# Kernel optimization log

Hardware: AMD Instinct MI355X
Metric: run time of the kernel (lower is better)

## Reference

```python
import jax, jax.numpy as jnp
import numpy as np

N_NODES = 40000
N_EDGES = 150000
H, D = 4, 128  # heads, per-head dim (h_feats=512)


def _edge_softmax(e, dst, n):
    # e: [E, H] attention logits; softmax over edges sharing a dst node
    m = jax.ops.segment_max(e, dst, num_segments=n)
    w = jnp.exp(e - m[dst])
    s = jax.ops.segment_sum(w, dst, num_segments=n)
    return w / s[dst]


def _gat_conv(x, src, dst, W, al, ar, b, activate):
    # DGL GATConv: feat = x @ W -> [N, H, D]
    n = x.shape[0]
    feat = (x @ W).reshape(n, H, D)
    el = jnp.einsum('nhd,hd->nh', feat, al)  # [N, H]
    er = jnp.einsum('nhd,hd->nh', feat, ar)
    e = jax.nn.leaky_relu(el[src] + er[dst], negative_slope=0.2)  # [E, H]
    a = _edge_softmax(e, dst, n)
    msg = feat[src] * a[:, :, None]  # [E, H, D]
    out = jax.ops.segment_sum(msg, dst, num_segments=n)  # [N, H, D]
    out = out + b.reshape(1, H, D)
    if activate:
        out = jax.nn.leaky_relu(out, negative_slope=0.01)  # F.leaky_relu default
    return out


def _hetero_layer(h, edges, W, al, ar, b, activate):
    # HeteroGraphConv with aggregate='sum' over edge types, then flatten heads
    n = h.shape[0]
    out = jnp.zeros((n, H, D), h.dtype)
    for t, (src, dst) in enumerate(edges):
        out = out + _gat_conv(h, src, dst, W[t], al[t], ar[t], b[t], activate)
    return out.reshape(n, H * D)


def setup_inputs() -> dict:
    key = jax.random.key(0)
    ks = jax.random.split(key, 20)
    inp = {}
    inp['x'] = jax.random.normal(ks[0], (N_NODES, 1024), jnp.float32)
    for i, nm in enumerate(['src0', 'dst0', 'src1', 'dst1']):
        inp[nm] = jax.random.randint(ks[1 + i], (N_EDGES,), 0, N_NODES, jnp.int32)
    def wscale(k, shape, fan_in):
        return jax.random.normal(k, shape, jnp.float32) * (1.0 / np.sqrt(fan_in))
    inp['W0'] = wscale(ks[5], (2, 1024, 512), 1024)
    inp['al0'] = wscale(ks[6], (2, H, D), D)
    inp['ar0'] = wscale(ks[7], (2, H, D), D)
    inp['b0'] = jnp.zeros((2, 512), jnp.float32)
    inp['W1'] = wscale(ks[8], (2, 512, 512), 512)
    inp['al1'] = wscale(ks[9], (2, H, D), D)
    inp['ar1'] = wscale(ks[10], (2, H, D), D)
    inp['b1'] = jnp.zeros((2, 512), jnp.float32)
    inp['W2'] = wscale(ks[11], (2, 512, 512), 512)
    inp['al2'] = wscale(ks[12], (2, H, D), D)
    inp['ar2'] = wscale(ks[13], (2, H, D), D)
    inp['b2'] = jnp.zeros((2, 512), jnp.float32)
    inp['Wout'] = wscale(ks[14], (512, 2983), 512)
    inp['bout'] = jnp.zeros((2983,), jnp.float32)
    return inp


def reference(x, src0, dst0, src1, dst1,
              W0, al0, ar0, b0, W1, al1, ar1, b1, W2, al2, ar2, b2,
              Wout, bout):
    edges = [(src0, dst0), (src1, dst1)]
    h = _hetero_layer(x, edges, W0, al0, ar0, b0, activate=True)
    h = _hetero_layer(h, edges, W1, al1, ar1, b1, activate=True)
    h = _hetero_layer(h, edges, W2, al2, ar2, b2, activate=False)
    return h @ Wout + bout
```

## Files before the change

kernel.cpp:

```cpp
#include <hip/hip_runtime.h>
#include <hip/hip_bf16.h>

#define NN 40000
#define NE 150000
#define HF 512
#define NHEAD 4

typedef __bf16 bf16x8 __attribute__((ext_vector_type(8)));
typedef float floatx4 __attribute__((ext_vector_type(4)));
typedef __hip_bfloat16 bf16;
typedef unsigned short u16;

__device__ __forceinline__ float bf2f(bf16 v) { return __bfloat162float(v); }
__device__ __forceinline__ float u2f(u16 v) { return __uint_as_float(((unsigned)v) << 16); }

__device__ __forceinline__ void gload16(const void* g, void* l) {
    __builtin_amdgcn_global_load_lds(
        (const __attribute__((address_space(1))) void*)g,
        (__attribute__((address_space(3))) void*)l, 16, 0, 0);
}

__device__ __forceinline__ void wait_vm0() {
    asm volatile("s_waitcnt vmcnt(0)" ::: "memory");
}

__device__ __forceinline__ void store_c(float* p, float v) { *p = v; }
__device__ __forceinline__ void store_c(bf16* p, float v) { *p = __float2bfloat16(v); }

__global__ void cast_k(const float* __restrict__ in, bf16* __restrict__ out, int n) {
    int i = (blockIdx.x * blockDim.x + threadIdx.x) * 8;
    if (i + 7 < n) {
        float4 v0 = *(const float4*)(in + i);
        float4 v1 = *(const float4*)(in + i + 4);
        union { uint4 u; u16 s[8]; } w;
        float fv[8] = {v0.x, v0.y, v0.z, v0.w, v1.x, v1.y, v1.z, v1.w};
#pragma unroll
        for (int j = 0; j < 8; j++) {
            bf16 b = __float2bfloat16(fv[j]);
            w.s[j] = *(const u16*)&b;
        }
        *(uint4*)(out + i) = w.u;
    } else {
        for (int j = i; j < n; j++) out[j] = __float2bfloat16(in[j]);
    }
}

__global__ void transpose_k(const float* __restrict__ W, bf16* __restrict__ WT,
                            int K, int Nn) {
    __shared__ float tile[32][33];
    int n0 = blockIdx.x * 32, k0 = blockIdx.y * 32;
    int tx = threadIdx.x, ty = threadIdx.y;
    int n = n0 + tx, k = k0 + ty;
    if (n < Nn && k < K) tile[ty][tx] = W[(size_t)k * Nn + n];
    __syncthreads();
    int nn = n0 + ty, kk = k0 + tx;
    if (nn < Nn && kk < K) WT[(size_t)nn * K + kk] = __float2bfloat16(tile[tx][ty]);
}

template <typename TOUT, bool HAS_BIAS>
__global__ __launch_bounds__(256) void gemm_k(const bf16* __restrict__ A,
                                              const bf16* __restrict__ BT,
                                              TOUT* __restrict__ C,
                                              const float* __restrict__ bias,
                                              int M, int Nn, int K) {
    __shared__ __align__(16) unsigned short As[2][128][32];
    __shared__ __align__(16) unsigned short Bs[2][128][32];

    const int nwg = gridDim.x * gridDim.y;
    const int orig = blockIdx.y * gridDim.x + blockIdx.x;
    const int qq = nwg >> 3, r8 = nwg & 7;
    const int xcd = orig & 7, loc = orig >> 3;
    const int swz = (xcd < r8 ? xcd * (qq + 1) : r8 * (qq + 1) + (xcd - r8) * qq) + loc;
    const int ntile = swz % gridDim.x;
    const int mtile = swz / gridDim.x;
    const int m0 = mtile * 128;
    const int n0 = ntile * 128;

    const int t = threadIdx.x;
    const int lane = t & 63;
    const int wave = t >> 6;
    const int wm = wave >> 1, wn = wave & 1;
    const int q = lane >> 4, r = lane & 15;

    const int srow = wave * 32 + (lane >> 2);
    const int scol = ((lane & 3) ^ ((srow >> 1) & 3)) * 8;
    int ar0 = m0 + srow;        if (ar0 >= M)  ar0 = M - 1;
    int ar1 = m0 + srow + 16;   if (ar1 >= M)  ar1 = M - 1;
    int br0 = n0 + srow;        if (br0 >= Nn) br0 = Nn - 1;
    int br1 = n0 + srow + 16;   if (br1 >= Nn) br1 = Nn - 1;
    const unsigned short* Ag0 = (const unsigned short*)A + (size_t)ar0 * K + scol;
    const unsigned short* Ag1 = (const unsigned short*)A + (size_t)ar1 * K + scol;
    const unsigned short* Bg0 = (const unsigned short*)BT + (size_t)br0 * K + scol;
    const unsigned short* Bg1 = (const unsigned short*)BT + (size_t)br1 * K + scol;
    unsigned short* Alb[2] = {&As[0][0][0] + wave * 1024, &As[1][0][0] + wave * 1024};
    unsigned short* Blb[2] = {&Bs[0][0][0] + wave * 1024, &Bs[1][0][0] + wave * 1024};

    const int rchunk = (q ^ ((r >> 1) & 3)) * 8;

    floatx4 acc[4][4] = {};
    const int nt = K >> 5;
    int cur = 0;
    gload16(Ag0, Alb[0]);
    gload16(Ag1, Alb[0] + 512);
    gload16(Bg0, Blb[0]);
    gload16(Bg1, Blb[0] + 512);
    wait_vm0();
    __syncthreads();
    for (int tt = 0; tt < nt; tt++) {
        if (tt + 1 < nt) {
            const int k1 = (tt + 1) << 5;
            gload16(Ag0 + k1, Alb[cur ^ 1]);
            gload16(Ag1 + k1, Alb[cur ^ 1] + 512);
            gload16(Bg0 + k1, Blb[cur ^ 1]);
            gload16(Bg1 + k1, Blb[cur ^ 1] + 512);
        }
        bf16x8 a[4], b[4];
#pragma unroll
        for (int i = 0; i < 4; i++)
            a[i] = *(const bf16x8*)&As[cur][wm * 64 + i * 16 + r][rchunk];
#pragma unroll
        for (int j = 0; j < 4; j++)
            b[j] = *(const bf16x8*)&Bs[cur][wn * 64 + j * 16 + r][rchunk];
#pragma unroll
        for (int i = 0; i < 4; i++)
#pragma unroll
            for (int j = 0; j < 4; j++)
                acc[i][j] = __builtin_amdgcn_mfma_f32_16x16x32_bf16(a[i], b[j], acc[i][j], 0, 0, 0);
        wait_vm0();
        __syncthreads();
        cur ^= 1;
    }

    float bv4[4] = {0.f, 0.f, 0.f, 0.f};
    if (HAS_BIAS) {
#pragma unroll
        for (int j = 0; j < 4; j++) {
            int col = n0 + wn * 64 + j * 16 + r;
            if (col < Nn) bv4[j] = bias[col];
        }
    }
#pragma unroll
    for (int i = 0; i < 4; i++)
#pragma unroll
        for (int j = 0; j < 4; j++)
#pragma unroll
            for (int rr = 0; rr < 4; rr++) {
                int row = m0 + wm * 64 + i * 16 + q * 4 + rr;
                int col = n0 + wn * 64 + j * 16 + r;
                if (row < M && col < Nn) {
                    float v = acc[i][j][rr];
                    if (HAS_BIAS) v += bv4[j];
                    store_c(&C[(size_t)row * Nn + col], v);
                }
            }
}

__global__ void attn_k(const bf16* __restrict__ featb, const float* __restrict__ al_l,
                       const float* __restrict__ ar_l, float* __restrict__ el,
                       float* __restrict__ er) {
    int lane = threadIdx.x & 63;
    int wave = threadIdx.x >> 6;
    int node = blockIdx.x * 4 + wave;
    if (node >= NN) return;
    int tt = lane >> 5, h = (lane >> 3) & 3, ld = lane & 7;
    const u16* fp = (const u16*)featb + (size_t)node * 1024 + lane * 16;
    union { uint4 v; u16 s[8]; } u0, u1;
    u0.v = *(const uint4*)fp;
    u1.v = *(const uint4*)(fp + 8);
    const float* alp = al_l + tt * HF + h * 128 + ld * 16;
    const float* arp = ar_l + tt * HF + h * 128 + ld * 16;
    float sl = 0.f, sr = 0.f;
#pragma unroll
    for (int j = 0; j < 8; j++) {
        float f = u2f(u0.s[j]);
        sl += f * alp[j];
        sr += f * arp[j];
    }
#pragma unroll
    for (int j = 0; j < 8; j++) {
        float f = u2f(u1.s[j]);
        sl += f * alp[8 + j];
        sr += f * arp[8 + j];
    }
#pragma unroll
    for (int off = 4; off >= 1; off >>= 1) {
        sl += __shfl_down(sl, off, 8);
        sr += __shfl_down(sr, off, 8);
    }
    if (ld == 0) {
        size_t o = (size_t)tt * NN * NHEAD + node * NHEAD + h;
        el[o] = sl;
        er[o] = sr;
    }
}

__global__ void deg_count_k(const int* __restrict__ dst, int* __restrict__ deg) {
    int e = blockIdx.x * blockDim.x + threadIdx.x;
    if (e < NE) atomicAdd(&deg[dst[e]], 1);
}

__global__ void scan_k(const int* __restrict__ deg, int* __restrict__ off) {
    __shared__ int part[1024];
    const int CH = (NN + 1023) >> 10;
    int t = threadIdx.x;
    int base = t * CH;
    int s = 0;
    for (int i = 0; i < CH; i++) {
        int idx = base + i;
        if (idx < NN) s += deg[idx];
    }
    part[t] = s;
    __syncthreads();
    for (int d = 1; d < 1024; d <<= 1) {
        int v = (t >= d) ? part[t - d] : 0;
        __syncthreads();
        part[t] += v;
        __syncthreads();
    }
    int run = (t == 0) ? 0 : part[t - 1];
    for (int i = 0; i < CH; i++) {
        int idx = base + i;
        if (idx < NN) {
            off[idx] = run;
            run += deg[idx];
        } else if (idx == NN) {
            off[NN] = run;
        }
    }
}

__global__ void fill_k(const int* __restrict__ src, const int* __restrict__ dst,
                       const int* __restrict__ off, int* __restrict__ cur,
                       int* __restrict__ csrc) {
    int e = blockIdx.x * blockDim.x + threadIdx.x;
    if (e >= NE) return;
    int d = dst[e];
    int p = atomicAdd(&cur[d], 1);
    csrc[off[d] + p] = src[e];
}

__global__ __launch_bounds__(256) void gather_k(
    const int* __restrict__ off0, const int* __restrict__ csrc0,
    const int* __restrict__ off1, const int* __restrict__ csrc1,
    const float* __restrict__ el, const float* __restrict__ er,
    const bf16* __restrict__ featb, const float* __restrict__ bb_l,
    bf16* __restrict__ hout, int act) {
    int lane = threadIdx.x & 63;
    int wave = threadIdx.x >> 6;
    int d = blockIdx.x * 4 + wave;
    if (d >= NN) return;
    int h = lane >> 4;
    const int* offs[2] = {off0, off1};
    const int* csrcs[2] = {csrc0, csrc1};

    float out[8] = {};
#pragma unroll
    for (int tt = 0; tt < 2; tt++) {
        const int* off = offs[tt];
        const int* csrc = csrcs[tt];
        const float* elt = el + (size_t)tt * NN * NHEAD;
        int o0 = off[d], o1 = off[d + 1];
        float erd = er[(size_t)tt * NN * NHEAD + d * NHEAD + h];
        float m = -3.0e38f, sum = 0.f;
        for (int i = o0; i < o1; i++) {
            int s = csrc[i];
            float lg = elt[s * NHEAD + h] + erd;
            lg = lg > 0.f ? lg : 0.2f * lg;
            float mn = fmaxf(m, lg);
            sum = sum * __expf(m - mn) + __expf(lg - mn);
            m = mn;
        }
        float inv = sum > 0.f ? 1.f / sum : 0.f;
        float acc[8] = {};
        for (int i = o0; i < o1; i++) {
            int s = csrc[i];
            float lg = elt[s * NHEAD + h] + erd;
            lg = lg > 0.f ? lg : 0.2f * lg;
            float a = __expf(lg - m) * inv;
            const u16* fp = (const u16*)featb + (size_t)s * 1024 + tt * HF + lane * 8;
            union { uint4 v; u16 s8[8]; } u;
            u.v = *(const uint4*)fp;
#pragma unroll
            for (int j = 0; j < 8; j++) acc[j] += u2f(u.s8[j]) * a;
        }
        const float* bp = bb_l + tt * HF + lane * 8;
        float4 b0 = *(const float4*)bp;
        float4 b1 = *(const float4*)(bp + 4);
        float bv[8] = {b0.x, b0.y, b0.z, b0.w, b1.x, b1.y, b1.z, b1.w};
#pragma unroll
        for (int j = 0; j < 8; j++) {
            float v = acc[j] + bv[j];
            if (act) v = v > 0.f ? v : 0.01f * v;
            out[j] += v;
        }
    }
    union { uint4 v; u16 s[8]; } outw;
#pragma unroll
    for (int j = 0; j < 8; j++) {
        bf16 ob = __float2bfloat16(out[j]);
        outw.s[j] = *(const u16*)&ob;
    }
    *(uint4*)((u16*)hout + (size_t)d * HF + lane * 8) = outw.v;
}

extern "C" void kernel_launch(void* const* d_in, const int* in_sizes, int n_in,
                              void* d_out, int out_size, void* d_ws, size_t ws_size,
                              hipStream_t stream) {
    const float* x = (const float*)d_in[0];
    const int* srcs[2] = {(const int*)d_in[1], (const int*)d_in[3]};
    const int* dsts[2] = {(const int*)d_in[2], (const int*)d_in[4]};
    const float* W[3] = {(const float*)d_in[5], (const float*)d_in[9], (const float*)d_in[13]};
    const float* al[3] = {(const float*)d_in[6], (const float*)d_in[10], (const float*)d_in[14]};
    const float* ar[3] = {(const float*)d_in[7], (const float*)d_in[11], (const float*)d_in[15]};
    const float* bb[3] = {(const float*)d_in[8], (const float*)d_in[12], (const float*)d_in[16]};
    const float* Wout = (const float*)d_in[17];
    const float* bout = (const float*)d_in[18];

    char* ws = (char*)d_ws;
    size_t off = 0;
    auto walloc = [&](size_t bytes) {
        void* p = ws + off;
        off = (off + bytes + 255) & ~(size_t)255;
        return p;
    };
    bf16* h0 = (bf16*)walloc((size_t)NN * HF * 2);
    bf16* h1 = (bf16*)walloc((size_t)NN * HF * 2);
    float* el = (float*)walloc((size_t)2 * NN * NHEAD * 4);
    float* er = (float*)walloc((size_t)2 * NN * NHEAD * 4);
    bf16* WT = (bf16*)walloc((size_t)2983 * 512 * 2);
    bf16* WT2 = (bf16*)walloc((size_t)1024 * 1024 * 2);
    int* deg = (int*)walloc((size_t)NN * 4);
    int* cur = (int*)walloc((size_t)NN * 4);
    int* offs[2];
    int* csrc[2];
    for (int t = 0; t < 2; t++) {
        offs[t] = (int*)walloc((size_t)(NN + 1) * 4);
        csrc[t] = (int*)walloc((size_t)NE * 4);
    }

    bf16* xb = (bf16*)((char*)d_out + (size_t)NN * HF * 4);
    bf16* featb = (bf16*)((char*)d_out + (size_t)NN * HF * 4 + (size_t)NN * 1024 * 2);

    cast_k<<<(NN * 1024 / 8 + 255) / 256, 256, 0, stream>>>(x, xb, NN * 1024);

    const int EB = (NE + 255) / 256;
    for (int t = 0; t < 2; t++) {
        hipMemsetAsync(deg, 0, (size_t)NN * 4, stream);
        hipMemsetAsync(cur, 0, (size_t)NN * 4, stream);
        deg_count_k<<<EB, 256, 0, stream>>>(dsts[t], deg);
        scan_k<<<1, 1024, 0, stream>>>(deg, offs[t]);
        fill_k<<<EB, 256, 0, stream>>>(srcs[t], dsts[t], offs[t], cur, csrc[t]);
    }

    const int MT = (NN + 127) / 128;

    for (int l = 0; l < 3; l++) {
        const int K = (l == 0) ? 1024 : 512;
        const bf16* hin = (l == 0) ? xb : ((l == 1) ? h0 : h1);
        bf16* hout = (l == 0) ? h0 : ((l == 1) ? h1 : h0);
        const int act = (l < 2) ? 1 : 0;
        for (int t = 0; t < 2; t++)
            transpose_k<<<dim3(512 / 32, K / 32), dim3(32, 32), 0, stream>>>(
                W[l] + (size_t)t * K * 512, WT2 + (size_t)t * 512 * K, K, 512);
        gemm_k<bf16, false><<<dim3(1024 / 128, MT), 256, 0, stream>>>(
            hin, WT2, featb, nullptr, NN, 1024, K);
        attn_k<<<NN / 4, 256, 0, stream>>>(featb, al[l], ar[l], el, er);
        gather_k<<<NN / 4, 256, 0, stream>>>(offs[0], csrc[0], offs[1], csrc[1],
                                             el, er, featb, bb[l], hout, act);
    }

    transpose_k<<<dim3((2983 + 31) / 32, 512 / 32), dim3(32, 32), 0, stream>>>(
        Wout, WT, 512, 2983);
    gemm_k<float, true><<<dim3((2983 + 127) / 128, MT), 256, 0, stream>>>(
        h0, WT, (float*)d_out, bout, NN, 2983, 512);
}
```

Before: 1.578 ms.

## Triple-buffer GEMM LDS tiles with partial vmcnt waits and nontemporal float stores

Turns the GEMM main loop from double to triple buffering. Loads are now issued two K-tiles ahead, and the loop waits only until the older tile has arrived (vmcnt(4)) instead of draining all loads each iteration. This aims to hide global-memory latency behind the MFMA work. It also switches float output stores to nontemporal stores to reduce cache pollution, at the cost of 50% more LDS per block, which may lower occupancy.

Result: slower. 1.726 ms (+9.4%).

```diff
diff --git a/kernel.cpp b/kernel.cpp
--- a/kernel.cpp
+++ b/kernel.cpp
@@ -20,11 +20,9 @@
         (__attribute__((address_space(3))) void*)l, 16, 0, 0);
 }
 
-__device__ __forceinline__ void wait_vm0() {
-    asm volatile("s_waitcnt vmcnt(0)" ::: "memory");
-}
-
-__device__ __forceinline__ void store_c(float* p, float v) { *p = v; }
+__device__ __forceinline__ void store_c(float* p, float v) {
+    __builtin_nontemporal_store(v, p);
+}
 __device__ __forceinline__ void store_c(bf16* p, float v) { *p = __float2bfloat16(v); }
 
 __global__ void cast_k(const float* __restrict__ in, bf16* __restrict__ out, int n) {
@@ -63,8 +61,8 @@
                                               TOUT* __restrict__ C,
                                               const float* __restrict__ bias,
                                               int M, int Nn, int K) {
-    __shared__ __align__(16) unsigned short As[2][128][32];
-    __shared__ __align__(16) unsigned short Bs[2][128][32];
+    __shared__ __align__(16) unsigned short As[3][128][32];
+    __shared__ __align__(16) unsigned short Bs[3][128][32];
 
     const int nwg = gridDim.x * gridDim.y;
     const int orig = blockIdx.y * gridDim.x + blockIdx.x;
@@ -92,27 +90,34 @@
     const unsigned short* Ag1 = (const unsigned short*)A + (size_t)ar1 * K + scol;
     const unsigned short* Bg0 = (const unsigned short*)BT + (size_t)br0 * K + scol;
     const unsigned short* Bg1 = (const unsigned short*)BT + (size_t)br1 * K + scol;
-    unsigned short* Alb[2] = {&As[0][0][0] + wave * 1024, &As[1][0][0] + wave * 1024};
-    unsigned short* Blb[2] = {&Bs[0][0][0] + wave * 1024, &Bs[1][0][0] + wave * 1024};
 
     const int rchunk = (q ^ ((r >> 1) & 3)) * 8;
+
+    unsigned short* Abase = &As[0][0][0] + wave * 1024;
+    unsigned short* Bbase = &Bs[0][0][0] + wave * 1024;
+
+    auto STAGE = [&](int kk, int buf) {
+        const int k1 = kk << 5;
+        unsigned short* Al = Abase + buf * 4096;
+        unsigned short* Bl = Bbase + buf * 4096;
+        gload16(Ag0 + k1, Al);
+        gload16(Ag1 + k1, Al + 512);
+        gload16(Bg0 + k1, Bl);
+        gload16(Bg1 + k1, Bl + 512);
+    };
 
     floatx4 acc[4][4] = {};
     const int nt = K >> 5;
+    STAGE(0, 0);
+    STAGE(1, 1);
+    asm volatile("s_waitcnt vmcnt(4)" ::: "memory");
+    __builtin_amdgcn_s_barrier();
     int cur = 0;
-    gload16(Ag0, Alb[0]);
-    gload16(Ag1, Alb[0] + 512);
-    gload16(Bg0, Blb[0]);
-    gload16(Bg1, Blb[0] + 512);
-    wait_vm0();
-    __syncthreads();
     for (int tt = 0; tt < nt; tt++) {
-        if (tt + 1 < nt) {
-            const int k1 = (tt + 1) << 5;
-            gload16(Ag0 + k1, Alb[cur ^ 1]);
-            gload16(Ag1 + k1, Alb[cur ^ 1] + 512);
-            gload16(Bg0 + k1, Blb[cur ^ 1]);
-            gload16(Bg1 + k1, Blb[cur ^ 1] + 512);
+        const bool pf = (tt + 2) < nt;
+        if (pf) {
+            int nb = cur + 2; if (nb >= 3) nb -= 3;
+            STAGE(tt + 2, nb);
         }
         bf16x8 a[4], b[4];
 #pragma unroll
@@ -126,9 +131,10 @@
 #pragma unroll
             for (int j = 0; j < 4; j++)
                 acc[i][j] = __builtin_amdgcn_mfma_f32_16x16x32_bf16(a[i], b[j], acc[i][j], 0, 0, 0);
-        wait_vm0();
-        __syncthreads();
-        cur ^= 1;
+        if (pf) asm volatile("s_waitcnt vmcnt(4) lgkmcnt(0)" ::: "memory");
+        else    asm volatile("s_waitcnt vmcnt(0) lgkmcnt(0)" ::: "memory");
+        __builtin_amdgcn_s_barrier();
+        cur = (cur == 2) ? 0 : cur + 1;
     }
 
     float bv4[4] = {0.f, 0.f, 0.f, 0.f};
```
